# Kernel optimization log

Measured on AMD Instinct MI355X. Metric: run time of the kernel, lower is better.

The kernel has to match this reference:

```python
import jax, jax.numpy as jnp
import numpy as np

B, G, N, P, E, F, K = 8, 256, 1024, 4, 1, 256, 4
ZERO_TOL = 1e-9
INF = 1e12
ATT_SLOPE = 0.2  # leaky relu slope inside attention


def setup_inputs() -> dict:
    key = jax.random.key(0)
    ks = jax.random.split(key, 6)
    stdv = float(1.0 / np.sqrt(G * P))
    x = jax.random.normal(ks[0], (B, G, N), jnp.float32)
    mixer = jax.random.uniform(ks[1], (P, E, 2 * F), jnp.float32, -stdv, stdv)
    weight = jax.random.uniform(ks[2], (P, E, F, G), jnp.float32, -stdv, stdv)
    weight_bias = jnp.zeros((P, E, F), jnp.float32)  # reset_parameters inits to 0
    filterWeight = jax.random.uniform(ks[3], (P, F, E, K, G), jnp.float32, -stdv, stdv)
    bias = jax.random.uniform(ks[4], (F, 1), jnp.float32, -stdv, stdv)
    adj = (jax.random.uniform(ks[5], (B, E, N, N)) < 0.05).astype(jnp.float32)
    S = jnp.maximum(adj, jnp.eye(N, dtype=jnp.float32)[None, None])
    return dict(x=x, mixer=mixer, weight=weight, weight_bias=weight_bias,
                filterWeight=filterWeight, bias=bias, S=S)


def reference(x, mixer, weight, weight_bias, filterWeight, bias, S):
    # --- learnAttentionGSOBatch ---
    # Wx: [B,P,E,F,N]
    Wx = jnp.einsum('pefg,bgn->bpefn', weight, x) + weight_bias[None, :, :, :, None]
    a1 = mixer[..., :F]   # [P,E,F]
    a2 = mixer[..., F:]   # [P,E,F]
    e1 = jnp.einsum('pef,bpefn->bpen', a1, Wx)  # a1^T W x_j
    e2 = jnp.einsum('pef,bpefn->bpen', a2, Wx)  # a2^T W x_i
    # aWx[b,p,e,i,j] = e1[j] + e2[i]  (matches a1Wx + a2Wx^T broadcast)
    aWx = e1[..., None, :] + e2[..., :, None]   # [B,P,E,N,N]
    eij = jax.nn.leaky_relu(aWx, ATT_SLOPE)
    mask = (jnp.sum(jnp.abs(S), axis=1)[:, None, None] > ZERO_TOL).astype(x.dtype)  # [B,1,1,N,N]
    aij = jax.nn.softmax(eij * mask - (1.0 - mask) * INF, axis=-1) * mask  # [B,P,E,N,N]

    # --- K-hop polynomial filter ---
    xk = jnp.broadcast_to(x[:, None, None], (B, P, E, G, N))
    zs = [xk]
    for _ in range(1, K):
        xk = jnp.matmul(xk, aij)        # diffuse along attention GSO
        zs.append(xk)
    z = jnp.stack(zs, axis=3)            # [B,P,E,K,G,N]
    # h reshape [P,F,E*K*G] contracted against z reshaped [B,P,N,E*K*G]
    y = jnp.einsum('bpekgn,pfekg->bpfn', z, filterWeight) + bias  # bias [F,1] broadcasts

    # --- forward wrapper: nonlinearity (leaky_relu, default slope 0.01) + head concat ---
    y = jax.nn.leaky_relu(y)                              # [B,P,F,N]
    y = jnp.transpose(y, (0, 3, 1, 2)).reshape(B, N, P * F)
    return jnp.transpose(y, (0, 2, 1))                    # [B, P*F, N]
```

## Files before the change

kernel.cpp:

```cpp
#include <hip/hip_runtime.h>
#include <hip/hip_bf16.h>

#define B_ 8
#define G_ 256
#define N_ 1024
#define P_ 4
#define F_ 256
#define KHOP 4
#define KG_ (KHOP * G_)

typedef unsigned short ushort_t;
typedef __bf16 bf16x8 __attribute__((ext_vector_type(8)));
typedef unsigned short u16x8 __attribute__((ext_vector_type(8)));
typedef float f32x4 __attribute__((ext_vector_type(4)));

__device__ __forceinline__ unsigned short f2bf(float f) {
  union { float fl; unsigned int i; } v; v.fl = f;
  return (unsigned short)((v.i + 0x7fffu + ((v.i >> 16) & 1u)) >> 16);
}

__device__ __forceinline__ void gload_lds16(const ushort_t* g, ushort_t* l) {
  __builtin_amdgcn_global_load_lds(
      (const __attribute__((address_space(1))) void*)g,
      (__attribute__((address_space(3))) void*)l, 16, 0, 0);
}

__global__ __launch_bounds__(256) void k_prep(
    const float* __restrict__ x, const float* __restrict__ mixer,
    const float* __restrict__ weight, const float* __restrict__ wb,
    const float* __restrict__ fw, float* __restrict__ e1, float* __restrict__ e2,
    ushort_t* __restrict__ fwbf, ushort_t* __restrict__ xT,
    float* __restrict__ sumb) {
  int blk = blockIdx.x;
  int t = threadIdx.x;
  if (blk < 128) {
    __shared__ float s1[G_], s2[G_];
    __shared__ float cred[2][4];
    int bp = blk >> 2;
    int nc = blk & 3;
    int b = bp >> 2, p = bp & (P_ - 1);
    int n = nc * 256 + t;
    float acc1 = 0.f, acc2 = 0.f;
    const float* wp = weight + (size_t)p * F_ * G_ + t;
    const float* mp = mixer + p * 2 * F_;
    for (int f = 0; f < F_; ++f) {
      float wv = wp[(size_t)f * G_];
      acc1 = fmaf(mp[f], wv, acc1);
      acc2 = fmaf(mp[F_ + f], wv, acc2);
    }
    s1[t] = acc1;
    s2[t] = acc2;
    float c1p = mp[t] * wb[p * F_ + t];
    float c2p = mp[F_ + t] * wb[p * F_ + t];
#pragma unroll
    for (int mask = 1; mask < 64; mask <<= 1) {
      c1p += __shfl_xor(c1p, mask, 64);
      c2p += __shfl_xor(c2p, mask, 64);
    }
    if ((t & 63) == 0) {
      cred[0][t >> 6] = c1p;
      cred[1][t >> 6] = c2p;
    }
    __syncthreads();
    float c1 = cred[0][0] + cred[0][1] + cred[0][2] + cred[0][3];
    float c2 = cred[1][0] + cred[1][1] + cred[1][2] + cred[1][3];
    const float* xb = x + (size_t)b * G_ * N_ + n;
    float a1 = 0.f, a2 = 0.f;
#pragma unroll 8
    for (int g = 0; g < G_; ++g) {
      float xv = xb[(size_t)g * N_];
      a1 = fmaf(s1[g], xv, a1);
      a2 = fmaf(s2[g], xv, a2);
    }
    e1[(size_t)bp * N_ + n] = c1 + a1;
    e2[(size_t)bp * N_ + n] = c2 + a2;
  } else if (blk < 128 + 1024) {
    int i = (blk - 128) * 1024 + t * 4;
    float4 v = *(const float4*)&fw[i];
    ushort4 o;
    o.x = f2bf(v.x); o.y = f2bf(v.y); o.z = f2bf(v.z); o.w = f2bf(v.w);
    *(ushort4*)&fwbf[i] = o;
  } else if (blk < 1152 + 512) {
    __shared__ ushort_t tile[64][66];
    int idx = blk - 1152;
    int n0 = (idx & 15) * 64;
    int g0 = ((idx >> 4) & 3) * 64;
    int b = idx >> 6;
    int rr = t >> 4, cc = (t & 15) * 4;
#pragma unroll
    for (int ps = 0; ps < 4; ++ps) {
      float4 v = *(const float4*)&x[((size_t)b * G_ + g0 + ps * 16 + rr) * N_ + n0 + cc];
      tile[ps * 16 + rr][cc] = f2bf(v.x);
      tile[ps * 16 + rr][cc + 1] = f2bf(v.y);
      tile[ps * 16 + rr][cc + 2] = f2bf(v.z);
      tile[ps * 16 + rr][cc + 3] = f2bf(v.w);
    }
    __syncthreads();
#pragma unroll
    for (int ps = 0; ps < 4; ++ps) {
      int nl = ps * 16 + rr;
      int gl = cc;
      ushort4 o;
      o.x = tile[gl][nl];
      o.y = tile[gl + 1][nl];
      o.z = tile[gl + 2][nl];
      o.w = tile[gl + 3][nl];
      *(ushort4*)&xT[((size_t)b * N_ + n0 + nl) * G_ + g0 + gl] = o;
    }
  } else {
    int i = (blk - 1664) * 256 + t;
    sumb[i] = 0.f;
  }
}

__global__ __launch_bounds__(256) void k_att(const float* __restrict__ e1,
                                             const float* __restrict__ e2,
                                             const float* __restrict__ S,
                                             ushort_t* __restrict__ expT,
                                             float* __restrict__ sumb) {
  __shared__ ushort_t tile[256][72];
  __shared__ float se1[256];
  __shared__ float se2[64];
  int bp = blockIdx.z;
  int b = bp >> 2;
  int i0 = blockIdx.y * 64;
  int jt = blockIdx.x;
  int j0 = jt * 256;
  int t = threadIdx.x;
  int rr = t >> 4;
  int cc4 = t & 15;
  int cc = cc4 * 4;

  se1[t] = e1[(size_t)bp * N_ + j0 + t];
  if (t < 64) se2[t] = e2[(size_t)bp * N_ + i0 + t];
  __syncthreads();

  const float* Sb = S + (size_t)b * N_ * N_;
  float re2[4];
#pragma unroll
  for (int ps = 0; ps < 4; ++ps) re2[ps] = se2[ps * 16 + rr];
  float psum[4] = {0.f, 0.f, 0.f, 0.f};
#pragma unroll
  for (int js = 0; js < 4; ++js) {
    float4 e1q = *(float4*)&se1[js * 64 + cc];
    float e1v[4] = {e1q.x, e1q.y, e1q.z, e1q.w};
#pragma unroll
    for (int ps = 0; ps < 4; ++ps) {
      int il = ps * 16 + rr;
      float4 s4 = *(const float4*)&Sb[(size_t)(i0 + il) * N_ + j0 + js * 64 + cc];
      float sv[4] = {s4.x, s4.y, s4.z, s4.w};
#pragma unroll
      for (int s = 0; s < 4; ++s) {
        float v = e1v[s] + re2[ps];
        float l = v >= 0.f ? v : 0.2f * v;
        bool m = fabsf(sv[s]) > 1e-9f;
        float e = m ? __expf(l) : 0.f;
        psum[ps] += e;
        tile[js * 64 + cc + s][il] = f2bf(e);
      }
    }
  }
#pragma unroll
  for (int mask = 1; mask < 16; mask <<= 1) {
#pragma unroll
    for (int ps = 0; ps < 4; ++ps) psum[ps] += __shfl_xor(psum[ps], mask, 64);
  }
  if (cc4 == 0) {
#pragma unroll
    for (int ps = 0; ps < 4; ++ps)
      atomicAdd(&sumb[(size_t)bp * N_ + i0 + ps * 16 + rr], psum[ps]);
  }
  __syncthreads();
  ushort_t* Tb = expT + (size_t)bp * N_ * N_;
  int jl0 = t >> 3;
  int ig = (t & 7) * 8;
#pragma unroll
  for (int pass = 0; pass < 8; ++pass) {
    int jl = pass * 32 + jl0;
    u16x8 v = *(const u16x8*)&tile[jl][ig];
    *(u16x8*)&Tb[(size_t)(j0 + jl) * N_ + i0 + ig] = v;
  }
}

__global__ __launch_bounds__(256, 2) void gemm_step(
    const ushort_t* __restrict__ Aprev, const ushort_t* __restrict__ Bt,
    const ushort_t* __restrict__ fwbf, const ushort_t* __restrict__ xT,
    const float* __restrict__ bias, const float* __restrict__ sumb,
    ushort_t* __restrict__ outb, float* __restrict__ outf,
    int kslice, int has_prev, int last) {
  __shared__ ushort_t As[2][2][128 * 32];
  __shared__ ushort_t Bs[2][2][128 * 32];
  int id = blockIdx.x;
  int xcd = id & 7;
  int slot = id >> 3;
  int bp = xcd * 4 + (slot >> 4);
  int inner = slot & 15;
  int m0 = (inner >> 3) * 128;
  int n0 = (inner & 7) * 128;
  int p = bp & (P_ - 1), b = bp >> 2;
  int t = threadIdx.x;
  int lane = t & 63;
  int w = t >> 6;
  int wm = w >> 1, wn = w & 1;
  int lr = lane & 15, quad = lane >> 4;
  int rowL = t >> 2;
  int colL = (t & 3) * 8;
  int ldsoff = (t & ~63) * 8;

  const ushort_t* A1 = has_prev
      ? Aprev + (size_t)bp * (F_ * N_) + (size_t)(m0 + rowL) * N_ + colL
      : (const ushort_t*)nullptr;
  const ushort_t* B1 = Bt + (size_t)bp * N_ * N_ + (size_t)(n0 + rowL) * N_ + colL;
  const ushort_t* A2 = fwbf + (size_t)p * (F_ * KG_) + (size_t)(m0 + rowL) * KG_ +
                       kslice * G_ + colL;
  const ushort_t* B2 = xT + (size_t)b * (N_ * G_) + (size_t)(n0 + rowL) * G_ + colL;

  const int ntA = has_prev ? (N_ / 64) : 0;
  const int NT = ntA + G_ / 64;

  f32x4 acc[4][4] = {};

  auto stage = [&](int buf, int it) {
    const ushort_t *Ab, *Bb;
    size_t ldA, ldB;
    int ko;
    if (it < ntA) {
      Ab = A1; ldA = N_; Bb = B1; ldB = N_; ko = it * 64;
    } else {
      Ab = A2; ldA = KG_; Bb = B2; ldB = G_; ko = (it - ntA) * 64;
    }
    gload_lds16(Ab + ko,                 &As[buf][0][ldsoff]);
    gload_lds16(Ab + 64 * ldA + ko,      &As[buf][0][2048 + ldsoff]);
    gload_lds16(Ab + ko + 32,            &As[buf][1][ldsoff]);
    gload_lds16(Ab + 64 * ldA + ko + 32, &As[buf][1][2048 + ldsoff]);
    gload_lds16(Bb + ko,                 &Bs[buf][0][ldsoff]);
    gload_lds16(Bb + 64 * ldB + ko,      &Bs[buf][0][2048 + ldsoff]);
    gload_lds16(Bb + ko + 32,            &Bs[buf][1][ldsoff]);
    gload_lds16(Bb + 64 * ldB + ko + 32, &Bs[buf][1][2048 + ldsoff]);
  };

  stage(0, 0);
  int buf = 0;
  for (int it = 0; it < NT; ++it) {
    if (it + 1 < NT) {
      stage(buf ^ 1, it + 1);
      asm volatile("s_waitcnt vmcnt(8)" ::: "memory");
    } else {
      asm volatile("s_waitcnt vmcnt(0)" ::: "memory");
    }
    __builtin_amdgcn_s_barrier();
    asm volatile("" ::: "memory");
#pragma unroll
    for (int c = 0; c < 2; ++c) {
      bf16x8 af[4], bfr[4];
#pragma unroll
      for (int mi = 0; mi < 4; ++mi)
        af[mi] = __builtin_bit_cast(bf16x8,
            *(const u16x8*)&As[buf][c][(wm * 64 + mi * 16 + lr) * 32 + quad * 8]);
#pragma unroll
      for (int ni = 0; ni < 4; ++ni)
        bfr[ni] = __builtin_bit_cast(bf16x8,
            *(const u16x8*)&Bs[buf][c][(wn * 64 + ni * 16 + lr) * 32 + quad * 8]);
#pragma unroll
      for (int mi = 0; mi < 4; ++mi)
#pragma unroll
        for (int ni = 0; ni < 4; ++ni)
          acc[mi][ni] = __builtin_amdgcn_mfma_f32_16x16x32_bf16(af[mi], bfr[ni], acc[mi][ni], 0, 0, 0);
    }
    asm volatile("" ::: "memory");
    __builtin_amdgcn_s_barrier();
    buf ^= 1;
  }

  if (last) {
    float* Ob = outf + (size_t)bp * (F_ * N_);
#pragma unroll
    for (int mi = 0; mi < 4; ++mi) {
      int fbase = m0 + wm * 64 + mi * 16 + quad * 4;
#pragma unroll
      for (int ni = 0; ni < 4; ++ni) {
        int n = n0 + wn * 64 + ni * 16 + lr;
#pragma unroll
        for (int r = 0; r < 4; ++r) {
          float v = acc[mi][ni][r] + bias[fbase + r];
          Ob[(size_t)(fbase + r) * N_ + n] = v >= 0.f ? v : 0.01f * v;
        }
      }
    }
  } else {
    ushort_t* Ob = outb + (size_t)bp * (F_ * N_);
    float iv[4];
#pragma unroll
    for (int ni = 0; ni < 4; ++ni)
      iv[ni] = 1.0f / sumb[(size_t)bp * N_ + n0 + wn * 64 + ni * 16 + lr];
#pragma unroll
    for (int mi = 0; mi < 4; ++mi) {
      int fbase = m0 + wm * 64 + mi * 16 + quad * 4;
#pragma unroll
      for (int ni = 0; ni < 4; ++ni) {
        int n = n0 + wn * 64 + ni * 16 + lr;
#pragma unroll
        for (int r = 0; r < 4; ++r)
          Ob[(size_t)(fbase + r) * N_ + n] = f2bf(acc[mi][ni][r] * iv[ni]);
      }
    }
  }
}

extern "C" void kernel_launch(void* const* d_in, const int* in_sizes, int n_in,
                              void* d_out, int out_size, void* d_ws, size_t ws_size,
                              hipStream_t stream) {
  const float* x = (const float*)d_in[0];
  const float* mixer = (const float*)d_in[1];
  const float* weight = (const float*)d_in[2];
  const float* wb = (const float*)d_in[3];
  const float* fw = (const float*)d_in[4];
  const float* bias = (const float*)d_in[5];
  const float* S = (const float*)d_in[6];
  float* out = (float*)d_out;

  char* ws = (char*)d_ws;
  size_t off = 0;
  auto take = [&](size_t bytes) -> char* {
    char* p = ws + off;
    off = (off + bytes + 255) & ~(size_t)255;
    return p;
  };
  float* e1 = (float*)take((size_t)B_ * P_ * N_ * 4);
  float* e2 = (float*)take((size_t)B_ * P_ * N_ * 4);
  float* sumb = (float*)take((size_t)B_ * P_ * N_ * 4);
  ushort_t* fwbf = (ushort_t*)take((size_t)P_ * F_ * KHOP * G_ * 2);
  ushort_t* xT = (ushort_t*)take((size_t)B_ * N_ * G_ * 2);
  ushort_t* expT = (ushort_t*)take((size_t)B_ * P_ * N_ * N_ * 2);
  ushort_t* sA = (ushort_t*)take((size_t)B_ * P_ * F_ * N_ * 2);
  ushort_t* sB = (ushort_t*)take((size_t)B_ * P_ * F_ * N_ * 2);

  k_prep<<<1792, 256, 0, stream>>>(x, mixer, weight, wb, fw, e1, e2, fwbf, xT, sumb);
  k_att<<<dim3(4, 16, 32), 256, 0, stream>>>(e1, e2, S, expT, sumb);

  gemm_step<<<512, 256, 0, stream>>>(nullptr, expT, fwbf, xT, bias, sumb, sA, nullptr, 3, 0, 0);
  gemm_step<<<512, 256, 0, stream>>>(sA, expT, fwbf, xT, bias, sumb, sB, nullptr, 2, 1, 0);
  gemm_step<<<512, 256, 0, stream>>>(sB, expT, fwbf, xT, bias, sumb, sA, nullptr, 1, 1, 0);
  gemm_step<<<512, 256, 0, stream>>>(sA, expT, fwbf, xT, bias, sumb, nullptr, out, 0, 1, 1);
}
```

Baseline: 232.4 us.

## Use triple-buffered K=32 LDS pipeline with XOR-swizzled columns in gemm_step

Replaces the double-buffered K=64 staging with a three-stage ring of K=32 tiles, issuing the load two iterations ahead right after a single barrier per iteration instead of two. Global-to-LDS column offsets and the fragment read offsets are XOR-swizzled by row to reduce LDS bank conflicts on the 16-byte fragment reads. Each iteration now does half the MFMA work, so barrier overhead per FLOP rises, but prefetch depth increases and the trailing barrier is removed.

```diff
diff --git a/kernel.cpp b/kernel.cpp
--- a/kernel.cpp
+++ b/kernel.cpp
@@ -188,8 +188,8 @@
     const float* __restrict__ bias, const float* __restrict__ sumb,
     ushort_t* __restrict__ outb, float* __restrict__ outf,
     int kslice, int has_prev, int last) {
-  __shared__ ushort_t As[2][2][128 * 32];
-  __shared__ ushort_t Bs[2][2][128 * 32];
+  __shared__ ushort_t As[3][128 * 32];
+  __shared__ ushort_t Bs[3][128 * 32];
   int id = blockIdx.x;
   int xcd = id & 7;
   int slot = id >> 3;
@@ -204,72 +204,68 @@
   int wm = w >> 1, wn = w & 1;
   int lr = lane & 15, quad = lane >> 4;
   int rowL = t >> 2;
-  int colL = (t & 3) * 8;
+  int colSw = ((t & 3) ^ (rowL & 3)) * 8;
   int ldsoff = (t & ~63) * 8;
 
   const ushort_t* A1 = has_prev
-      ? Aprev + (size_t)bp * (F_ * N_) + (size_t)(m0 + rowL) * N_ + colL
+      ? Aprev + (size_t)bp * (F_ * N_) + (size_t)(m0 + rowL) * N_ + colSw
       : (const ushort_t*)nullptr;
-  const ushort_t* B1 = Bt + (size_t)bp * N_ * N_ + (size_t)(n0 + rowL) * N_ + colL;
+  const ushort_t* B1 = Bt + (size_t)bp * N_ * N_ + (size_t)(n0 + rowL) * N_ + colSw;
   const ushort_t* A2 = fwbf + (size_t)p * (F_ * KG_) + (size_t)(m0 + rowL) * KG_ +
-                       kslice * G_ + colL;
-  const ushort_t* B2 = xT + (size_t)b * (N_ * G_) + (size_t)(n0 + rowL) * G_ + colL;
-
-  const int ntA = has_prev ? (N_ / 64) : 0;
-  const int NT = ntA + G_ / 64;
+                       kslice * G_ + colSw;
+  const ushort_t* B2 = xT + (size_t)b * (N_ * G_) + (size_t)(n0 + rowL) * G_ + colSw;
+
+  const int ntA2 = has_prev ? (N_ / 32) : 0;
+  const int NT2 = ntA2 + G_ / 32;
 
   f32x4 acc[4][4] = {};
 
-  auto stage = [&](int buf, int it) {
+  auto stage = [&](int it, int buf) {
     const ushort_t *Ab, *Bb;
     size_t ldA, ldB;
     int ko;
-    if (it < ntA) {
-      Ab = A1; ldA = N_; Bb = B1; ldB = N_; ko = it * 64;
+    if (it < ntA2) {
+      Ab = A1; ldA = N_; Bb = B1; ldB = N_; ko = it * 32;
     } else {
-      Ab = A2; ldA = KG_; Bb = B2; ldB = G_; ko = (it - ntA) * 64;
-    }
-    gload_lds16(Ab + ko,                 &As[buf][0][ldsoff]);
-    gload_lds16(Ab + 64 * ldA + ko,      &As[buf][0][2048 + ldsoff]);
-    gload_lds16(Ab + ko + 32,            &As[buf][1][ldsoff]);
-    gload_lds16(Ab + 64 * ldA + ko + 32, &As[buf][1][2048 + ldsoff]);
-    gload_lds16(Bb + ko,                 &Bs[buf][0][ldsoff]);
-    gload_lds16(Bb + 64 * ldB + ko,      &Bs[buf][0][2048 + ldsoff]);
-    gload_lds16(Bb + ko + 32,            &Bs[buf][1][ldsoff]);
-    gload_lds16(Bb + 64 * ldB + ko + 32, &Bs[buf][1][2048 + ldsoff]);
+      Ab = A2; ldA = KG_; Bb = B2; ldB = G_; ko = (it - ntA2) * 32;
+    }
+    gload_lds16(Ab + ko,                 &As[buf][ldsoff]);
+    gload_lds16(Ab + 64 * ldA + ko,      &As[buf][2048 + ldsoff]);
+    gload_lds16(Bb + ko,                 &Bs[buf][ldsoff]);
+    gload_lds16(Bb + 64 * ldB + ko,      &Bs[buf][2048 + ldsoff]);
   };
 
   stage(0, 0);
-  int buf = 0;
-  for (int it = 0; it < NT; ++it) {
-    if (it + 1 < NT) {
-      stage(buf ^ 1, it + 1);
-      asm volatile("s_waitcnt vmcnt(8)" ::: "memory");
-    } else {
+  stage(1, 1);
+  int cur = 0;
+  int qA = (quad ^ (lr & 3)) * 8;
+  for (int it = 0; it < NT2; ++it) {
+    if (it < NT2 - 1)
+      asm volatile("s_waitcnt vmcnt(4)" ::: "memory");
+    else
       asm volatile("s_waitcnt vmcnt(0)" ::: "memory");
-    }
     __builtin_amdgcn_s_barrier();
-    asm volatile("" ::: "memory");
-#pragma unroll
-    for (int c = 0; c < 2; ++c) {
+    if (it + 2 < NT2) {
+      int stg = cur + 2; if (stg >= 3) stg -= 3;
+      stage(it + 2, stg);
+    }
+    {
       bf16x8 af[4], bfr[4];
 #pragma unroll
       for (int mi = 0; mi < 4; ++mi)
         af[mi] = __builtin_bit_cast(bf16x8,
-            *(const u16x8*)&As[buf][c][(wm * 64 + mi * 16 + lr) * 32 + quad * 8]);
+            *(const u16x8*)&As[cur][(wm * 64 + mi * 16 + lr) * 32 + qA]);
 #pragma unroll
       for (int ni = 0; ni < 4; ++ni)
         bfr[ni] = __builtin_bit_cast(bf16x8,
-            *(const u16x8*)&Bs[buf][c][(wn * 64 + ni * 16 + lr) * 32 + quad * 8]);
+            *(const u16x8*)&Bs[cur][(wn * 64 + ni * 16 + lr) * 32 + qA]);
 #pragma unroll
       for (int mi = 0; mi < 4; ++mi)
 #pragma unroll
         for (int ni = 0; ni < 4; ++ni)
           acc[mi][ni] = __builtin_amdgcn_mfma_f32_16x16x32_bf16(af[mi], bfr[ni], acc[mi][ni], 0, 0, 0);
     }
-    asm volatile("" ::: "memory");
-    __builtin_amdgcn_s_barrier();
-    buf ^= 1;
+    cur = cur + 1; if (cur == 3) cur = 0;
   }
 
   if (last) {
```

Measured after the change: 245.6 us. 1.06x slower.

## Use 256x128 GEMM tiles with 8 waves and MFMA-fragment-ordered LDS layout

Applied to the files above, without the earlier changes.

Each gemm_step block now covers the full F=256 rows with 512 threads (8 waves), so every loaded expT/B tile is reused across all 256 output rows rather than being fetched by two separate blocks. The grid halves to 256 blocks. LDS is rearranged so that each wave's 16-row by 32-col fragment is stored contiguously in lane order, which makes the fragment reads simple lane*8 offsets and is meant to avoid bank conflicts. The cost is fewer blocks on a large GPU, less latency hiding, and double the LDS per block.

```diff
diff --git a/kernel.cpp b/kernel.cpp
--- a/kernel.cpp
+++ b/kernel.cpp
@@ -182,101 +182,120 @@
   }
 }
 
-__global__ __launch_bounds__(256, 2) void gemm_step(
+__global__ __launch_bounds__(512, 2) void gemm_step(
     const ushort_t* __restrict__ Aprev, const ushort_t* __restrict__ Bt,
     const ushort_t* __restrict__ fwbf, const ushort_t* __restrict__ xT,
     const float* __restrict__ bias, const float* __restrict__ sumb,
     ushort_t* __restrict__ outb, float* __restrict__ outf,
     int kslice, int has_prev, int last) {
-  __shared__ ushort_t As[2][2][128 * 32];
-  __shared__ ushort_t Bs[2][2][128 * 32];
+  __shared__ ushort_t As[2][16384];
+  __shared__ ushort_t Bs[2][8192];
   int id = blockIdx.x;
   int xcd = id & 7;
   int slot = id >> 3;
-  int bp = xcd * 4 + (slot >> 4);
-  int inner = slot & 15;
-  int m0 = (inner >> 3) * 128;
-  int n0 = (inner & 7) * 128;
+  int bp = xcd * 4 + (slot >> 3);
+  int n0 = (slot & 7) * 128;
   int p = bp & (P_ - 1), b = bp >> 2;
   int t = threadIdx.x;
   int lane = t & 63;
   int w = t >> 6;
   int wm = w >> 1, wn = w & 1;
   int lr = lane & 15, quad = lane >> 4;
-  int rowL = t >> 2;
-  int colL = (t & 3) * 8;
-  int ldsoff = (t & ~63) * 8;
-
-  const ushort_t* A1 = has_prev
-      ? Aprev + (size_t)bp * (F_ * N_) + (size_t)(m0 + rowL) * N_ + colL
-      : (const ushort_t*)nullptr;
-  const ushort_t* B1 = Bt + (size_t)bp * N_ * N_ + (size_t)(n0 + rowL) * N_ + colL;
-  const ushort_t* A2 = fwbf + (size_t)p * (F_ * KG_) + (size_t)(m0 + rowL) * KG_ +
-                       kslice * G_ + colL;
-  const ushort_t* B2 = xT + (size_t)b * (N_ * G_) + (size_t)(n0 + rowL) * G_ + colL;
+
+  int rowA[4], colA[4];
+#pragma unroll
+  for (int l = 0; l < 4; ++l) {
+    int cell = l * 8 + w;
+    rowA[l] = (cell >> 1) * 16 + lr;
+    colA[l] = (cell & 1) * 32 + quad * 8;
+  }
+  int rowB[2], colB[2];
+#pragma unroll
+  for (int l = 0; l < 2; ++l) {
+    int cell = l * 8 + w;
+    rowB[l] = (cell >> 1) * 16 + lr;
+    colB[l] = (cell & 1) * 32 + quad * 8;
+  }
+
+  const ushort_t* Abase1 = has_prev ? (Aprev + (size_t)bp * (F_ * N_)) : fwbf;
+  const ushort_t* Abase2 = fwbf + (size_t)p * (F_ * KG_) + (size_t)kslice * G_;
+  const ushort_t* Bbase1 = Bt + (size_t)bp * N_ * N_;
+  const ushort_t* Bbase2 = xT + (size_t)b * (N_ * G_);
+
+  const ushort_t* pA1[4]; const ushort_t* pA2[4];
+  const ushort_t* pB1[2]; const ushort_t* pB2[2];
+#pragma unroll
+  for (int l = 0; l < 4; ++l) {
+    pA1[l] = Abase1 + (size_t)rowA[l] * N_ + colA[l];
+    pA2[l] = Abase2 + (size_t)rowA[l] * KG_ + colA[l];
+  }
+#pragma unroll
+  for (int l = 0; l < 2; ++l) {
+    pB1[l] = Bbase1 + (size_t)(n0 + rowB[l]) * N_ + colB[l];
+    pB2[l] = Bbase2 + (size_t)(n0 + rowB[l]) * G_ + colB[l];
+  }
 
   const int ntA = has_prev ? (N_ / 64) : 0;
   const int NT = ntA + G_ / 64;
 
   f32x4 acc[4][4] = {};
 
-  auto stage = [&](int buf, int it) {
-    const ushort_t *Ab, *Bb;
-    size_t ldA, ldB;
-    int ko;
+  auto stage = [&](int it, int buf) {
     if (it < ntA) {
-      Ab = A1; ldA = N_; Bb = B1; ldB = N_; ko = it * 64;
+      int ko = it * 64;
+#pragma unroll
+      for (int l = 0; l < 4; ++l)
+        gload_lds16(pA1[l] + ko, &As[buf][l * 4096 + w * 512]);
+#pragma unroll
+      for (int l = 0; l < 2; ++l)
+        gload_lds16(pB1[l] + ko, &Bs[buf][l * 4096 + w * 512]);
     } else {
-      Ab = A2; ldA = KG_; Bb = B2; ldB = G_; ko = (it - ntA) * 64;
-    }
-    gload_lds16(Ab + ko,                 &As[buf][0][ldsoff]);
-    gload_lds16(Ab + 64 * ldA + ko,      &As[buf][0][2048 + ldsoff]);
-    gload_lds16(Ab + ko + 32,            &As[buf][1][ldsoff]);
-    gload_lds16(Ab + 64 * ldA + ko + 32, &As[buf][1][2048 + ldsoff]);
-    gload_lds16(Bb + ko,                 &Bs[buf][0][ldsoff]);
-    gload_lds16(Bb + 64 * ldB + ko,      &Bs[buf][0][2048 + ldsoff]);
-    gload_lds16(Bb + ko + 32,            &Bs[buf][1][ldsoff]);
-    gload_lds16(Bb + 64 * ldB + ko + 32, &Bs[buf][1][2048 + ldsoff]);
+      int ko = (it - ntA) * 64;
+#pragma unroll
+      for (int l = 0; l < 4; ++l)
+        gload_lds16(pA2[l] + ko, &As[buf][l * 4096 + w * 512]);
+#pragma unroll
+      for (int l = 0; l < 2; ++l)
+        gload_lds16(pB2[l] + ko, &Bs[buf][l * 4096 + w * 512]);
+    }
   };
 
   stage(0, 0);
-  int buf = 0;
+  int cur = 0;
   for (int it = 0; it < NT; ++it) {
     if (it + 1 < NT) {
-      stage(buf ^ 1, it + 1);
-      asm volatile("s_waitcnt vmcnt(8)" ::: "memory");
+      stage(it + 1, cur ^ 1);
+      asm volatile("s_waitcnt vmcnt(6)" ::: "memory");
     } else {
       asm volatile("s_waitcnt vmcnt(0)" ::: "memory");
     }
     __builtin_amdgcn_s_barrier();
-    asm volatile("" ::: "memory");
 #pragma unroll
     for (int c = 0; c < 2; ++c) {
       bf16x8 af[4], bfr[4];
 #pragma unroll
       for (int mi = 0; mi < 4; ++mi)
         af[mi] = __builtin_bit_cast(bf16x8,
-            *(const u16x8*)&As[buf][c][(wm * 64 + mi * 16 + lr) * 32 + quad * 8]);
+            *(const u16x8*)&As[cur][((wm * 4 + mi) * 2 + c) * 512 + lane * 8]);
 #pragma unroll
       for (int ni = 0; ni < 4; ++ni)
         bfr[ni] = __builtin_bit_cast(bf16x8,
-            *(const u16x8*)&Bs[buf][c][(wn * 64 + ni * 16 + lr) * 32 + quad * 8]);
+            *(const u16x8*)&Bs[cur][((wn * 4 + ni) * 2 + c) * 512 + lane * 8]);
 #pragma unroll
       for (int mi = 0; mi < 4; ++mi)
 #pragma unroll
         for (int ni = 0; ni < 4; ++ni)
           acc[mi][ni] = __builtin_amdgcn_mfma_f32_16x16x32_bf16(af[mi], bfr[ni], acc[mi][ni], 0, 0, 0);
     }
-    asm volatile("" ::: "memory");
     __builtin_amdgcn_s_barrier();
-    buf ^= 1;
+    cur ^= 1;
   }
 
   if (last) {
     float* Ob = outf + (size_t)bp * (F_ * N_);
 #pragma unroll
     for (int mi = 0; mi < 4; ++mi) {
-      int fbase = m0 + wm * 64 + mi * 16 + quad * 4;
+      int fbase = wm * 64 + mi * 16 + quad * 4;
 #pragma unroll
       for (int ni = 0; ni < 4; ++ni) {
         int n = n0 + wn * 64 + ni * 16 + lr;
@@ -295,7 +314,7 @@
       iv[ni] = 1.0f / sumb[(size_t)bp * N_ + n0 + wn * 64 + ni * 16 + lr];
 #pragma unroll
     for (int mi = 0; mi < 4; ++mi) {
-      int fbase = m0 + wm * 64 + mi * 16 + quad * 4;
+      int fbase = wm * 64 + mi * 16 + quad * 4;
 #pragma unroll
       for (int ni = 0; ni < 4; ++ni) {
         int n = n0 + wn * 64 + ni * 16 + lr;
@@ -338,8 +357,8 @@
   k_prep<<<1792, 256, 0, stream>>>(x, mixer, weight, wb, fw, e1, e2, fwbf, xT, sumb);
   k_att<<<dim3(4, 16, 32), 256, 0, stream>>>(e1, e2, S, expT, sumb);
 
-  gemm_step<<<512, 256, 0, stream>>>(nullptr, expT, fwbf, xT, bias, sumb, sA, nullptr, 3, 0, 0);
-  gemm_step<<<512, 256, 0, stream>>>(sA, expT, fwbf, xT, bias, sumb, sB, nullptr, 2, 1, 0);
-  gemm_step<<<512, 256, 0, stream>>>(sB, expT, fwbf, xT, bias, sumb, sA, nullptr, 1, 1, 0);
-  gemm_step<<<512, 256, 0, stream>>>(sA, expT, fwbf, xT, bias, sumb, nullptr, out, 0, 1, 1);
-}
+  gemm_step<<<256, 512, 0, stream>>>(nullptr, expT, fwbf, xT, bias, sumb, sA, nullptr, 3, 0, 0);
+  gemm_step<<<256, 512, 0, stream>>>(sA, expT, fwbf, xT, bias, sumb, sB, nullptr, 2, 1, 0);
+  gemm_step<<<256, 512, 0, stream>>>(sB, expT, fwbf, xT, bias, sumb, sA, nullptr, 1, 1, 0);
+  gemm_step<<<256, 512, 0, stream>>>(sA, expT, fwbf, xT, bias, sumb, nullptr, out, 0, 1, 1);
+}
```

Result: slower. 286.4 us (+23.2%).
